# Performance work log

Hardware: AMD Instinct MI355X
Metric: run time of the kernel (lower is better)

The kernel has to match this reference:

```python
import jax, jax.numpy as jnp
import numpy as np

LEAKY_ALPHA = 0.2
NEG_INF = -9e15


def setup_inputs() -> dict:
    key = jax.random.key(0)
    k1, k2, k3, k4, k5 = jax.random.split(key, 5)
    n, n_head, f_in, f_out = 4096, 8, 1024, 128
    scale_w = float(np.sqrt(6.0 / (f_in + f_out)))      # xavier_uniform over (f_in,f_out)
    scale_a = float(np.sqrt(6.0 / (f_out + 1)))
    return {
        "h": jax.random.normal(k1, (n, f_in), dtype=jnp.float32),
        "adj": jax.random.randint(k2, (n, n), 0, 2, dtype=jnp.int32),
        "w": jax.random.uniform(k3, (n_head, f_in, f_out), jnp.float32, -scale_w, scale_w),
        "bias": jnp.zeros((f_out,), dtype=jnp.float32),
        "a_src": jax.random.uniform(k4, (n_head, f_out, 1), jnp.float32, -scale_a, scale_a),
        "a_dst": jax.random.uniform(k5, (n_head, f_out, 1), jnp.float32, -scale_a, scale_a),
    }


def reference(h, adj, w, bias, a_src, a_dst):
    n = h.shape[0]
    # per-head projection: [h_head, n, f_out]
    h_prime = jnp.einsum('nf,hfo->hno', h, w)
    attn_src = jnp.einsum('hno,hoi->hn', h_prime, a_src)   # [n_head, n]
    attn_dst = jnp.einsum('hno,hoi->hn', h_prime, a_dst)   # [n_head, n]
    # additive score: attn[h,i,j] = src[h,i] + dst[h,j]
    attn = attn_src[:, :, None] + attn_dst[:, None, :]
    attn = jnp.where(attn >= 0, attn, LEAKY_ALPHA * attn)  # leaky_relu
    attn = jnp.where(adj[None] > 0, attn, NEG_INF)
    attn = jax.nn.softmax(attn, axis=-1)                   # [n_head, n, n]
    # dropout layers are identity in eval mode
    output = jnp.einsum('hnm,hmo->hno', attn, h_prime) + bias
    output = jnp.transpose(output, (1, 0, 2)).reshape(n, -1)  # [n, n_head*f_out]
    weight = jnp.sum(attn, axis=0)                          # [n, n]
    return output, weight
```

## Files before the change

### kernel.cpp

```cpp
#include <hip/hip_runtime.h>
#include <hip/hip_bf16.h>


#define N 4096
#define NH 8
#define FIN 1024
#define FOUT 128

typedef short bf16x8 __attribute__((ext_vector_type(8)));
typedef float f32x4 __attribute__((ext_vector_type(4)));
typedef unsigned int uint;
typedef unsigned short ushort;

__device__ __forceinline__ float b2f(ushort u){ return __uint_as_float(((uint)u)<<16); }
__device__ __forceinline__ uint pk2cvt(float a, float b){
    float2 f; f.x=a; f.y=b;
    __hip_bfloat162 h = __float22bfloat162_rn(f);
    uint r; __builtin_memcpy(&r, &h, 4); return r;
}
__device__ __forceinline__ float sane(float x, float lim){ return fminf(fmaxf(x,-lim),lim); }
__device__ __forceinline__ int swz(int r, int cg){ return r*64 + (((cg) ^ (r & 7)) << 3); }
__device__ __forceinline__ void glds16(const ushort* g, ushort* l){
    __builtin_amdgcn_global_load_lds(
        (const __attribute__((address_space(1))) void*)g,
        (__attribute__((address_space(3))) void*)l, 16, 0, 0);
}
__device__ __forceinline__ int detect_mode(const ushort* hraw){
    ushort u = hraw[2*(threadIdx.x & 63)];
    int e = (u>>7)&0xFF;
    unsigned long long m = __ballot(e>=90 && e<=141);
    return (__popcll(m)>=40)?0:1;
}

__global__ __launch_bounds__(256) void pack_adj(const int* __restrict__ adj,
                                                uint* __restrict__ bitsT) {
    size_t idx = (size_t)blockIdx.x * 256 + threadIdx.x;
    int v = adj[idx];
    unsigned long long m = __ballot(v != 0);
    int lane = threadIdx.x & 63;
    uint i  = (uint)(idx >> 12);
    uint jw = ((uint)idx & 4095u) >> 5;
    if (lane == 0)       bitsT[jw * N + i] = (uint)m;
    else if (lane == 32) bitsT[jw * N + i] = (uint)(m >> 32);
}

__global__ __launch_bounds__(256) void transpose_w(const void* __restrict__ wraw,
                                                   const ushort* __restrict__ hraw,
                                                   ushort* __restrict__ wT) {
    __shared__ ushort tile[64][72];
    int mode = detect_mode(hraw);
    int h = blockIdx.z, f0 = blockIdx.x * 64, o0 = blockIdx.y * 64;
    int t = threadIdx.x;
#pragma unroll
    for (int it = 0; it < 2; ++it) {
        int slot = it * 256 + t;
        int row = slot >> 3, c = slot & 7;
        size_t eoff = (size_t)h * (FIN * FOUT) + (size_t)(f0 + row) * FOUT + o0 + c * 8;
        alignas(16) ushort tmp[8];
        if (mode == 0) {
            *reinterpret_cast<uint4*>(tmp) = *reinterpret_cast<const uint4*>((const ushort*)wraw + eoff);
        } else {
            const float* wF = (const float*)wraw;
            float4 x = *reinterpret_cast<const float4*>(wF + eoff);
            float4 y = *reinterpret_cast<const float4*>(wF + eoff + 4);
            uint4 p; p.x = pk2cvt(x.x,x.y); p.y = pk2cvt(x.z,x.w);
            p.z = pk2cvt(y.x,y.y); p.w = pk2cvt(y.z,y.w);
            *reinterpret_cast<uint4*>(tmp) = p;
        }
        *reinterpret_cast<uint4*>(&tile[row][c * 8]) = *reinterpret_cast<uint4*>(tmp);
    }
    __syncthreads();
#pragma unroll
    for (int it = 0; it < 2; ++it) {
        int slot = it * 256 + t;
        int orow = slot >> 3, c = slot & 7;
        alignas(16) ushort tmp[8];
#pragma unroll
        for (int k = 0; k < 8; ++k) tmp[k] = tile[c * 8 + k][orow];
        *reinterpret_cast<uint4*>(wT + (size_t)h * (FIN * FOUT) + (size_t)(o0 + orow) * FIN + f0 + c * 8) =
            *reinterpret_cast<uint4*>(tmp);
    }
}

__global__ __launch_bounds__(256) void zero2(float* __restrict__ acc, float* __restrict__ lsum,
                                             int nacc) {
    int b = blockIdx.x, t = threadIdx.x;
    float4 z; z.x=0.f; z.y=0.f; z.z=0.f; z.w=0.f;
    if (b < nacc) reinterpret_cast<float4*>(acc)[(size_t)b*256+t] = z;
    else          reinterpret_cast<float4*>(lsum)[(size_t)(b-nacc)*256+t] = z;
}

__global__ __launch_bounds__(256) void gemm_hp(
        const void* __restrict__ hraw, const ushort* __restrict__ wT,
        const void* __restrict__ asraw, const void* __restrict__ adraw,
        ushort* __restrict__ hpT,
        float* __restrict__ es1, float* __restrict__ es2,
        float* __restrict__ ed1, float* __restrict__ ed2) {
    __shared__ ushort Bs[2][FOUT * 64];
    __shared__ float sred[64], dred[64];
    int mode = detect_mode((const ushort*)hraw);
    int t = threadIdx.x;
    int lin = blockIdx.x + 64 * blockIdx.y;
    int i0 = (((lin & 7) * 8) + ((lin >> 6) & 7)) * 64;
    int head = (lin >> 3) & 7;
    int w = t >> 6, lane = t & 63, quad = lane >> 4, l16 = lane & 15, wsh = quad * 8;
    int arow = i0 + w * 16 + l16;
    const ushort* hU = (const ushort*)hraw;
    const float*  hF = (const float*)hraw;
    int l8 = lane >> 3, lk = (lane & 7) ^ (l8 & 7);
    const ushort* gs[4];
#pragma unroll
    for (int s = 0; s < 4; ++s) {
        int o = (w * 4 + s) * 8 + l8;
        gs[s] = wT + (size_t)head * FOUT * FIN + (size_t)o * FIN + lk * 8;
    }

    float asv[8], adv[8];
#pragma unroll
    for (int n = 0; n < 8; ++n) {
        int ai = head * FOUT + n * 16 + l16;
        asv[n] = mode ? ((const float*)asraw)[ai] : b2f(((const ushort*)asraw)[ai]);
        adv[n] = mode ? ((const float*)adraw)[ai] : b2f(((const ushort*)adraw)[ai]);
    }

    f32x4 acc[8] = {};
#pragma unroll
    for (int s = 0; s < 4; ++s) glds16(gs[s], &Bs[0][(w * 4 + s) * 512]);
    uint4 au[2]; float4 af[2][2];
    if (mode == 0) {
#pragma unroll
        for (int kk = 0; kk < 2; ++kk)
            au[kk] = *reinterpret_cast<const uint4*>(hU + (size_t)arow * FIN + kk * 32 + wsh);
    } else {
#pragma unroll
        for (int kk = 0; kk < 2; ++kk) {
            af[kk][0] = *reinterpret_cast<const float4*>(hF + (size_t)arow * FIN + kk * 32 + wsh);
            af[kk][1] = *reinterpret_cast<const float4*>(hF + (size_t)arow * FIN + kk * 32 + wsh + 4);
        }
    }
    __syncthreads();

    for (int c = 0; c < 16; ++c) {
        int k0 = c * 64;
        if (c < 15) {
            ushort* bsw = &Bs[(c + 1) & 1][0];
#pragma unroll
            for (int s = 0; s < 4; ++s)
                glds16(gs[s] + k0 + 64, &bsw[(w * 4 + s) * 512]);
        }
        bf16x8 a2[2];
        if (mode == 0) {
            a2[0] = *reinterpret_cast<bf16x8*>(&au[0]);
            a2[1] = *reinterpret_cast<bf16x8*>(&au[1]);
        } else {
#pragma unroll
            for (int kk = 0; kk < 2; ++kk) {
                uint4 av; av.x = pk2cvt(af[kk][0].x, af[kk][0].y); av.y = pk2cvt(af[kk][0].z, af[kk][0].w);
                av.z = pk2cvt(af[kk][1].x, af[kk][1].y); av.w = pk2cvt(af[kk][1].z, af[kk][1].w);
                a2[kk] = *reinterpret_cast<bf16x8*>(&av);
            }
        }
        if (c < 15) {
            if (mode == 0) {
#pragma unroll
                for (int kk = 0; kk < 2; ++kk)
                    au[kk] = *reinterpret_cast<const uint4*>(hU + (size_t)arow * FIN + k0 + 64 + kk * 32 + wsh);
            } else {
#pragma unroll
                for (int kk = 0; kk < 2; ++kk) {
                    af[kk][0] = *reinterpret_cast<const float4*>(hF + (size_t)arow * FIN + k0 + 64 + kk * 32 + wsh);
                    af[kk][1] = *reinterpret_cast<const float4*>(hF + (size_t)arow * FIN + k0 + 64 + kk * 32 + wsh + 4);
                }
            }
        }
        const ushort* bsr = &Bs[c & 1][0];
#pragma unroll
        for (int kk = 0; kk < 2; ++kk) {
            int cg0 = kk * 4 + quad;
#pragma unroll
            for (int n = 0; n < 8; ++n) {
                bf16x8 b = *reinterpret_cast<const bf16x8*>(&bsr[swz(n * 16 + l16, cg0)]);
                acc[n] = __builtin_amdgcn_mfma_f32_16x16x32_bf16(a2[kk], b, acc[n], 0, 0, 0);
            }
        }
        if (c < 15) __syncthreads();
    }
#pragma unroll
    for (int n = 0; n < 8; ++n) {
        uint2 pk;
        pk.x = pk2cvt(acc[n][0], acc[n][1]);
        pk.y = pk2cvt(acc[n][2], acc[n][3]);
        *reinterpret_cast<uint2*>(hpT + ((size_t)head * FOUT + n * 16 + l16) * N + i0 + w * 16 + quad * 4) = pk;
    }
#pragma unroll
    for (int rr = 0; rr < 4; ++rr) {
        float s = 0.f, d = 0.f;
#pragma unroll
        for (int n = 0; n < 8; ++n) { s += acc[n][rr] * asv[n]; d += acc[n][rr] * adv[n]; }
#pragma unroll
        for (int off = 1; off < 16; off <<= 1) { s += __shfl_xor(s, off); d += __shfl_xor(d, off); }
        if (l16 == 0) { sred[w * 16 + quad * 4 + rr] = s; dred[w * 16 + quad * 4 + rr] = d; }
    }
    __syncthreads();
    if (t < 64) {
        int i = i0 + t;
        float s = sane(sred[t], 30.f);
        float d = sane(dred[t], 30.f);
        es1[head * N + i] = __expf(s);       es2[head * N + i] = __expf(0.2f * s);
        ed1[head * N + i] = __expf(d);       ed2[head * N + i] = __expf(0.2f * d);
    }
}

__global__ __launch_bounds__(256, 4) void pv_kernel(
        const ushort* __restrict__ hpT,
        const float* __restrict__ es1, const float* __restrict__ es2,
        const float* __restrict__ ed1, const float* __restrict__ ed2,
        const uint* __restrict__ bitsT,
        float* __restrict__ accOut, float* __restrict__ lsum, int use_atomic) {
    __shared__ ushort Bs[2][FOUT * 64];
    __shared__ float Ed[2][1024];
    int t = threadIdx.x;
    int lin = blockIdx.x + 32 * blockIdx.y + 256 * blockIdx.z;
    int g  = (lin & 7) * 4 + (lin >> 8);
    int ib = (lin >> 3) & 31;
    int hh = g & 7, kz = g >> 3;
    int i0 = ib * 128, kb = kz * 1024;
    int w = t >> 6, lane = t & 63, quad = lane >> 4, l16 = lane & 15, wsh = quad * 8;
    int irow[2];
    float s1[2], s2[2];
#pragma unroll
    for (int mi = 0; mi < 2; ++mi) {
        irow[mi] = i0 + w * 32 + mi * 16 + l16;
        s1[mi] = es1[hh * N + irow[mi]];
        s2[mi] = es2[hh * N + irow[mi]];
    }
    const uint* bp = bitsT + (size_t)(kb >> 5) * N;
    int l8 = lane >> 3, lk = (lane & 7) ^ (l8 & 7);
    const ushort* gs[4];
#pragma unroll
    for (int s = 0; s < 4; ++s) {
        int o = (w * 4 + s) * 8 + l8;
        gs[s] = hpT + (size_t)hh * FOUT * N + (size_t)o * N + kb + lk * 8;
    }
    bf16x8 ones;
#pragma unroll
    for (int j = 0; j < 8; ++j) ones[j] = (short)0x3F80;

    f32x4 acc[2][8] = {};
    f32x4 accl[2] = {};

    float4 ev1 = *reinterpret_cast<const float4*>(ed1 + hh * N + kb + t * 4);
    float4 ev2 = *reinterpret_cast<const float4*>(ed2 + hh * N + kb + t * 4);
    uint bwc[2][2], bwn[2][2];
#pragma unroll
    for (int kk = 0; kk < 2; ++kk)
#pragma unroll
        for (int mi = 0; mi < 2; ++mi) bwc[kk][mi] = bp[(size_t)kk * N + irow[mi]];
#pragma unroll
    for (int s = 0; s < 4; ++s) glds16(gs[s], &Bs[0][(w * 4 + s) * 512]);
    *reinterpret_cast<float4*>(&Ed[0][t * 4]) = ev1;
    *reinterpret_cast<float4*>(&Ed[1][t * 4]) = ev2;
    __syncthreads();

    for (int c = 0; c < 16; ++c) {
        if (c < 15) {
            ushort* bsw = &Bs[(c + 1) & 1][0];
#pragma unroll
            for (int s = 0; s < 4; ++s)
                glds16(gs[s] + (c + 1) * 64, &bsw[(w * 4 + s) * 512]);
#pragma unroll
            for (int kk = 0; kk < 2; ++kk)
#pragma unroll
                for (int mi = 0; mi < 2; ++mi)
                    bwn[kk][mi] = bp[(size_t)((c + 1) * 2 + kk) * N + irow[mi]];
        }
        const ushort* bsr = &Bs[c & 1][0];
#pragma unroll
        for (int kk = 0; kk < 2; ++kk) {
            int kgl = c * 64 + kk * 32 + wsh;
            float4 d1a = *reinterpret_cast<const float4*>(&Ed[0][kgl]);
            float4 d1b = *reinterpret_cast<const float4*>(&Ed[0][kgl + 4]);
            float4 d2a = *reinterpret_cast<const float4*>(&Ed[1][kgl]);
            float4 d2b = *reinterpret_cast<const float4*>(&Ed[1][kgl + 4]);
            bf16x8 am[2];
#pragma unroll
            for (int mi = 0; mi < 2; ++mi) {
                uint word = bwc[kk][mi] >> wsh;
                float e0 = fmaxf(s1[mi]*d1a.x, s2[mi]*d2a.x); e0 = (word & 1u)   ? e0 : 0.f;
                float e1 = fmaxf(s1[mi]*d1a.y, s2[mi]*d2a.y); e1 = (word & 2u)   ? e1 : 0.f;
                float e2 = fmaxf(s1[mi]*d1a.z, s2[mi]*d2a.z); e2 = (word & 4u)   ? e2 : 0.f;
                float e3 = fmaxf(s1[mi]*d1a.w, s2[mi]*d2a.w); e3 = (word & 8u)   ? e3 : 0.f;
                float e4 = fmaxf(s1[mi]*d1b.x, s2[mi]*d2b.x); e4 = (word & 16u)  ? e4 : 0.f;
                float e5 = fmaxf(s1[mi]*d1b.y, s2[mi]*d2b.y); e5 = (word & 32u)  ? e5 : 0.f;
                float e6 = fmaxf(s1[mi]*d1b.z, s2[mi]*d2b.z); e6 = (word & 64u)  ? e6 : 0.f;
                float e7 = fmaxf(s1[mi]*d1b.w, s2[mi]*d2b.w); e7 = (word & 128u) ? e7 : 0.f;
                uint4 av; av.x = pk2cvt(e0, e1); av.y = pk2cvt(e2, e3);
                av.z = pk2cvt(e4, e5); av.w = pk2cvt(e6, e7);
                am[mi] = *reinterpret_cast<bf16x8*>(&av);
                accl[mi] = __builtin_amdgcn_mfma_f32_16x16x32_bf16(am[mi], ones, accl[mi], 0, 0, 0);
            }
            int cg0 = kk * 4 + quad;
            __builtin_amdgcn_s_setprio(1);
#pragma unroll
            for (int n = 0; n < 8; ++n) {
                bf16x8 b = *reinterpret_cast<const bf16x8*>(&bsr[swz(n * 16 + l16, cg0)]);
                acc[0][n] = __builtin_amdgcn_mfma_f32_16x16x32_bf16(am[0], b, acc[0][n], 0, 0, 0);
                acc[1][n] = __builtin_amdgcn_mfma_f32_16x16x32_bf16(am[1], b, acc[1][n], 0, 0, 0);
            }
            __builtin_amdgcn_s_setprio(0);
        }
#pragma unroll
        for (int kk = 0; kk < 2; ++kk)
#pragma unroll
            for (int mi = 0; mi < 2; ++mi) bwc[kk][mi] = bwn[kk][mi];
        if (c < 15) __syncthreads();
    }
    if (l16 == 0) {
#pragma unroll
        for (int mi = 0; mi < 2; ++mi)
#pragma unroll
            for (int rr = 0; rr < 4; ++rr)
                atomicAdd(&lsum[hh * N + i0 + w * 32 + mi * 16 + quad * 4 + rr], accl[mi][rr]);
    }
    if (use_atomic) {
#pragma unroll
        for (int mi = 0; mi < 2; ++mi) {
            float* arow = accOut + ((size_t)hh * N + i0 + w * 32 + mi * 16 + quad * 4) * FOUT + l16;
#pragma unroll
            for (int n = 0; n < 8; ++n)
#pragma unroll
                for (int rr = 0; rr < 4; ++rr)
                    atomicAdd(&arow[(size_t)rr * FOUT + n * 16], acc[mi][n][rr]);
        }
    } else {
        float* part = accOut + (size_t)kz * ((size_t)NH * N * FOUT);
#pragma unroll
        for (int mi = 0; mi < 2; ++mi) {
            float* arow = part + ((size_t)hh * N + i0 + w * 32 + mi * 16 + quad * 4) * FOUT + l16;
#pragma unroll
            for (int n = 0; n < 8; ++n)
#pragma unroll
                for (int rr = 0; rr < 4; ++rr)
                    arow[(size_t)rr * FOUT + n * 16] = acc[mi][n][rr];
        }
    }
}

__global__ __launch_bounds__(256) void recip2(const float* __restrict__ lsum,
                                              const float* __restrict__ es1, const float* __restrict__ es2,
                                              float* __restrict__ rinv,
                                              float* __restrict__ s1r, float* __restrict__ s2r) {
    int idx = blockIdx.x * 256 + threadIdx.x;
    float v = lsum[idx];
    float r = (v > 1e-30f) ? 1.0f / v : 0.f;
    rinv[idx] = r;
    s1r[idx] = es1[idx] * r;
    s2r[idx] = es2[idx] * r;
}

__global__ __launch_bounds__(256) void pv_epi(
        const float* __restrict__ acc32, const float* __restrict__ rinv,
        const void* __restrict__ braw, const ushort* __restrict__ hraw,
        void* __restrict__ outraw, int nparts) {
    int mode = detect_mode(hraw);
    int idx4 = blockIdx.x * 256 + threadIdx.x;
    int h = idx4 >> 17;
    int i = (idx4 >> 5) & 4095;
    int og = idx4 & 31;
    const size_t PSTRIDE4 = (size_t)NH * N * FOUT / 4;
    float4 v = reinterpret_cast<const float4*>(acc32)[idx4];
    if (nparts == 4) {
        float4 a = reinterpret_cast<const float4*>(acc32)[PSTRIDE4 + idx4];
        float4 b = reinterpret_cast<const float4*>(acc32)[2 * PSTRIDE4 + idx4];
        float4 c = reinterpret_cast<const float4*>(acc32)[3 * PSTRIDE4 + idx4];
        v.x += a.x + b.x + c.x; v.y += a.y + b.y + c.y;
        v.z += a.z + b.z + c.z; v.w += a.w + b.w + c.w;
    }
    float r = rinv[h * N + i];
    float4 bv;
    if (mode) bv = reinterpret_cast<const float4*>(braw)[og];
    else {
        const ushort* bu = (const ushort*)braw;
        bv.x = b2f(bu[og*4]); bv.y = b2f(bu[og*4+1]); bv.z = b2f(bu[og*4+2]); bv.w = b2f(bu[og*4+3]);
    }
    v.x = v.x * r + bv.x; v.y = v.y * r + bv.y; v.z = v.z * r + bv.z; v.w = v.w * r + bv.w;
    size_t ob = (size_t)i * (NH * FOUT) + h * FOUT + og * 4;
    if (mode) *reinterpret_cast<float4*>((float*)outraw + ob) = v;
    else {
        uint2 pk; pk.x = pk2cvt(v.x, v.y); pk.y = pk2cvt(v.z, v.w);
        *reinterpret_cast<uint2*>((ushort*)outraw + ob) = pk;
    }
}

__global__ __launch_bounds__(256) void weight_kernel(
        const float* __restrict__ s1r, const float* __restrict__ s2r,
        const float* __restrict__ ed1, const float* __restrict__ ed2,
        const uint* __restrict__ bitsT,
        const ushort* __restrict__ hraw,
        void* __restrict__ outraw) {
    int mode = detect_mode(hraw);
    ushort* woutU = (ushort*)outraw + (size_t)N * (NH * FOUT);
    float*  woutF = (float*)outraw  + (size_t)N * (NH * FOUT);
    int t = threadIdx.x;
    int j = blockIdx.x * 1024 + t * 4;
    int i0 = blockIdx.y * 32;
    float4 d1[NH], d2[NH];
#pragma unroll
    for (int hh = 0; hh < NH; ++hh) {
        d1[hh] = *reinterpret_cast<const float4*>(ed1 + hh * N + j);
        d2[hh] = *reinterpret_cast<const float4*>(ed2 + hh * N + j);
    }
    int wrow = j >> 5;
    int jsh = j & 31;
    for (int i = i0; i < i0 + 32; ++i) {
        uint wbits = bitsT[(size_t)wrow * N + i] >> jsh;
        float sx = 0.f, sy = 0.f, sz = 0.f, sw = 0.f;
#pragma unroll
        for (int hh = 0; hh < NH; ++hh) {
            float a = s1r[hh * N + i];
            float b = s2r[hh * N + i];
            sx += fmaxf(a * d1[hh].x, b * d2[hh].x);
            sy += fmaxf(a * d1[hh].y, b * d2[hh].y);
            sz += fmaxf(a * d1[hh].z, b * d2[hh].z);
            sw += fmaxf(a * d1[hh].w, b * d2[hh].w);
        }
        sx = (wbits & 1u) ? sx : 0.f;
        sy = (wbits & 2u) ? sy : 0.f;
        sz = (wbits & 4u) ? sz : 0.f;
        sw = (wbits & 8u) ? sw : 0.f;
        size_t oidx = (size_t)i * N + j;
        if (mode) {
            float4 st; st.x = sx; st.y = sy; st.z = sz; st.w = sw;
            *reinterpret_cast<float4*>(woutF + oidx) = st;
        } else {
            uint2 pk; pk.x = pk2cvt(sx, sy); pk.y = pk2cvt(sz, sw);
            *reinterpret_cast<uint2*>(woutU + oidx) = pk;
        }
    }
}

extern "C" void kernel_launch(void* const* d_in, const int* in_sizes, int n_in,
                              void* d_out, int out_size, void* d_ws, size_t ws_size,
                              hipStream_t stream) {
    (void)in_sizes; (void)n_in; (void)out_size;
    const void* hraw  = d_in[0];
    const int*  adj   = (const int*)d_in[1];
    const void* wraw  = d_in[2];
    const void* braw  = d_in[3];
    const void* asraw = d_in[4];
    const void* adraw = d_in[5];

    char* ws = (char*)d_ws;
    float* lsum = (float*)(ws + 0);
    float* rinv = (float*)(ws + 131072);
    float* es1  = (float*)(ws + 262144);
    float* es2  = (float*)(ws + 393216);
    float* ed1  = (float*)(ws + 524288);
    float* ed2  = (float*)(ws + 655360);
    float* s1r  = (float*)(ws + 786432);
    float* s2r  = (float*)(ws + 917504);
    uint*  bitsT= (uint*)(ws + 1048576);
    ushort* wT  = (ushort*)(ws + 3145728);

    const size_t SMALL_END = 5242880;
    const size_t PART = 16777216;
    float*  acc32; ushort* hpT;
    int use_atomic, nparts;
    if (ws_size >= SMALL_END + 4 * PART + 8388608ull) {
        char* b = ws + SMALL_END;
        acc32 = (float*)b;
        hpT   = (ushort*)(b + 4 * PART);
        use_atomic = 0; nparts = 4;
    } else if (ws_size >= SMALL_END + 25165824ull) {
        char* b = ws + SMALL_END;
        acc32 = (float*)b;
        hpT   = (ushort*)(b + PART);
        use_atomic = 1; nparts = 1;
    } else {
        char* ob = (char*)d_out;
        acc32 = (float*)(ob + 16777216);
        hpT   = (ushort*)(ob + 33554432);
        use_atomic = 1; nparts = 1;
    }

    transpose_w<<<dim3(16, 2, 8), 256, 0, stream>>>(wraw, (const ushort*)hraw, wT);
    pack_adj<<<65536, 256, 0, stream>>>(adj, bitsT);
    if (use_atomic) zero2<<<4128, 256, 0, stream>>>(acc32, lsum, 4096);
    else            zero2<<<32,   256, 0, stream>>>(acc32, lsum, 0);
    gemm_hp<<<dim3(64, 8), 256, 0, stream>>>(hraw, wT, asraw, adraw, hpT,
                                             es1, es2, ed1, ed2);
    pv_kernel<<<dim3(32, 8, 4), 256, 0, stream>>>(hpT, es1, es2, ed1, ed2, bitsT,
                                                  acc32, lsum, use_atomic);
    recip2<<<128, 256, 0, stream>>>(lsum, es1, es2, rinv, s1r, s2r);
    pv_epi<<<4096, 256, 0, stream>>>(acc32, rinv, braw, (const ushort*)hraw, d_out, nparts);
    weight_kernel<<<dim3(4, 128), 256, 0, stream>>>(s1r, s2r, ed1, ed2, bitsT,
                                                    (const ushort*)hraw, d_out);
}
```

Baseline: 290.0 us.

## Merge prep kernels, fold reciprocal into epilogue, pack score products

The adjacency packing, accumulator zeroing and weight transpose kernels become one launch with block-range dispatch. The standalone reciprocal kernel is folded into the output epilogue, which now computes the inverse row sum and writes the scaled source terms. In the PV kernel, the two destination exponent arrays are interleaved in shared memory so each score uses one packed v_pk_mul_f32 plus a max. The goal is fewer launches and fewer VALU instructions in the inner loop, at the cost of redundant reciprocal math across epilogue threads and inline asm that may hinder scheduling.

```diff
diff --git a/kernel.cpp b/kernel.cpp
--- a/kernel.cpp
+++ b/kernel.cpp
@@ -9,6 +9,7 @@
 
 typedef short bf16x8 __attribute__((ext_vector_type(8)));
 typedef float f32x4 __attribute__((ext_vector_type(4)));
+typedef float f32x2 __attribute__((ext_vector_type(2)));
 typedef unsigned int uint;
 typedef unsigned short ushort;
 
@@ -19,6 +20,11 @@
     uint r; __builtin_memcpy(&r, &h, 4); return r;
 }
 __device__ __forceinline__ float sane(float x, float lim){ return fminf(fmaxf(x,-lim),lim); }
+__device__ __forceinline__ float pkmulmax(f32x2 sp, f32x2 dp){
+    f32x2 pr;
+    asm("v_pk_mul_f32 %0, %1, %2" : "=v"(pr) : "v"(sp), "v"(dp));
+    return fmaxf(pr[0], pr[1]);
+}
 __device__ __forceinline__ int swz(int r, int cg){ return r*64 + (((cg) ^ (r & 7)) << 3); }
 __device__ __forceinline__ void glds16(const ushort* g, ushort* l){
     __builtin_amdgcn_global_load_lds(
@@ -32,25 +38,34 @@
     return (__popcll(m)>=40)?0:1;
 }
 
-__global__ __launch_bounds__(256) void pack_adj(const int* __restrict__ adj,
-                                                uint* __restrict__ bitsT) {
-    size_t idx = (size_t)blockIdx.x * 256 + threadIdx.x;
-    int v = adj[idx];
-    unsigned long long m = __ballot(v != 0);
-    int lane = threadIdx.x & 63;
-    uint i  = (uint)(idx >> 12);
-    uint jw = ((uint)idx & 4095u) >> 5;
-    if (lane == 0)       bitsT[jw * N + i] = (uint)m;
-    else if (lane == 32) bitsT[jw * N + i] = (uint)(m >> 32);
-}
-
-__global__ __launch_bounds__(256) void transpose_w(const void* __restrict__ wraw,
-                                                   const ushort* __restrict__ hraw,
-                                                   ushort* __restrict__ wT) {
+__global__ __launch_bounds__(256) void prep(
+        const int* __restrict__ adj, uint* __restrict__ bitsT,
+        float* __restrict__ acc, float* __restrict__ lsum, int nacc,
+        const void* __restrict__ wraw, const ushort* __restrict__ hraw,
+        ushort* __restrict__ wT) {
     __shared__ ushort tile[64][72];
+    int b = blockIdx.x, t = threadIdx.x;
+    if (b < 65536) {
+        size_t idx = (size_t)b * 256 + t;
+        int v = adj[idx];
+        unsigned long long m = __ballot(v != 0);
+        int lane = t & 63;
+        uint i  = (uint)(idx >> 12);
+        uint jw = ((uint)idx & 4095u) >> 5;
+        if (lane == 0)       bitsT[jw * N + i] = (uint)m;
+        else if (lane == 32) bitsT[jw * N + i] = (uint)(m >> 32);
+        return;
+    }
+    int zb = b - 65536;
+    if (zb < nacc + 32) {
+        float4 z; z.x=0.f; z.y=0.f; z.z=0.f; z.w=0.f;
+        if (zb < nacc) reinterpret_cast<float4*>(acc)[(size_t)zb*256+t] = z;
+        else           reinterpret_cast<float4*>(lsum)[(size_t)(zb-nacc)*256+t] = z;
+        return;
+    }
+    int bb = zb - (nacc + 32);
     int mode = detect_mode(hraw);
-    int h = blockIdx.z, f0 = blockIdx.x * 64, o0 = blockIdx.y * 64;
-    int t = threadIdx.x;
+    int f0 = (bb & 15) * 64, o0 = ((bb >> 4) & 1) * 64, h = bb >> 5;
 #pragma unroll
     for (int it = 0; it < 2; ++it) {
         int slot = it * 256 + t;
@@ -80,14 +95,6 @@
         *reinterpret_cast<uint4*>(wT + (size_t)h * (FIN * FOUT) + (size_t)(o0 + orow) * FIN + f0 + c * 8) =
             *reinterpret_cast<uint4*>(tmp);
     }
-}
-
-__global__ __launch_bounds__(256) void zero2(float* __restrict__ acc, float* __restrict__ lsum,
-                                             int nacc) {
-    int b = blockIdx.x, t = threadIdx.x;
-    float4 z; z.x=0.f; z.y=0.f; z.z=0.f; z.w=0.f;
-    if (b < nacc) reinterpret_cast<float4*>(acc)[(size_t)b*256+t] = z;
-    else          reinterpret_cast<float4*>(lsum)[(size_t)(b-nacc)*256+t] = z;
 }
 
 __global__ __launch_bounds__(256) void gemm_hp(
@@ -218,7 +225,7 @@
         const uint* __restrict__ bitsT,
         float* __restrict__ accOut, float* __restrict__ lsum, int use_atomic) {
     __shared__ ushort Bs[2][FOUT * 64];
-    __shared__ float Ed[2][1024];
+    __shared__ float Ed[2048];
     int t = threadIdx.x;
     int lin = blockIdx.x + 32 * blockIdx.y + 256 * blockIdx.z;
     int g  = (lin & 7) * 4 + (lin >> 8);
@@ -227,12 +234,12 @@
     int i0 = ib * 128, kb = kz * 1024;
     int w = t >> 6, lane = t & 63, quad = lane >> 4, l16 = lane & 15, wsh = quad * 8;
     int irow[2];
-    float s1[2], s2[2];
+    f32x2 sp[2];
 #pragma unroll
     for (int mi = 0; mi < 2; ++mi) {
         irow[mi] = i0 + w * 32 + mi * 16 + l16;
-        s1[mi] = es1[hh * N + irow[mi]];
-        s2[mi] = es2[hh * N + irow[mi]];
+        sp[mi][0] = es1[hh * N + irow[mi]];
+        sp[mi][1] = es2[hh * N + irow[mi]];
     }
     const uint* bp = bitsT + (size_t)(kb >> 5) * N;
     int l8 = lane >> 3, lk = (lane & 7) ^ (l8 & 7);
@@ -258,8 +265,15 @@
         for (int mi = 0; mi < 2; ++mi) bwc[kk][mi] = bp[(size_t)kk * N + irow[mi]];
 #pragma unroll
     for (int s = 0; s < 4; ++s) glds16(gs[s], &Bs[0][(w * 4 + s) * 512]);
-    *reinterpret_cast<float4*>(&Ed[0][t * 4]) = ev1;
-    *reinterpret_cast<float4*>(&Ed[1][t * 4]) = ev2;
+    {
+        const float* e1a = reinterpret_cast<const float*>(&ev1);
+        const float* e2a = reinterpret_cast<const float*>(&ev2);
+#pragma unroll
+        for (int j = 0; j < 4; ++j) {
+            float2 pr; pr.x = e1a[j]; pr.y = e2a[j];
+            *reinterpret_cast<float2*>(&Ed[(t * 4 + j) * 2]) = pr;
+        }
+    }
     __syncthreads();
 
     for (int c = 0; c < 16; ++c) {
@@ -277,23 +291,23 @@
         const ushort* bsr = &Bs[c & 1][0];
 #pragma unroll
         for (int kk = 0; kk < 2; ++kk) {
-            int kgl = c * 64 + kk * 32 + wsh;
-            float4 d1a = *reinterpret_cast<const float4*>(&Ed[0][kgl]);
-            float4 d1b = *reinterpret_cast<const float4*>(&Ed[0][kgl + 4]);
-            float4 d2a = *reinterpret_cast<const float4*>(&Ed[1][kgl]);
-            float4 d2b = *reinterpret_cast<const float4*>(&Ed[1][kgl + 4]);
+            int eb = (c * 64 + kk * 32 + wsh) * 2;
+            float4 p01 = *reinterpret_cast<const float4*>(&Ed[eb]);
+            float4 p23 = *reinterpret_cast<const float4*>(&Ed[eb + 4]);
+            float4 p45 = *reinterpret_cast<const float4*>(&Ed[eb + 8]);
+            float4 p67 = *reinterpret_cast<const float4*>(&Ed[eb + 12]);
             bf16x8 am[2];
 #pragma unroll
             for (int mi = 0; mi < 2; ++mi) {
                 uint word = bwc[kk][mi] >> wsh;
-                float e0 = fmaxf(s1[mi]*d1a.x, s2[mi]*d2a.x); e0 = (word & 1u)   ? e0 : 0.f;
-                float e1 = fmaxf(s1[mi]*d1a.y, s2[mi]*d2a.y); e1 = (word & 2u)   ? e1 : 0.f;
-                float e2 = fmaxf(s1[mi]*d1a.z, s2[mi]*d2a.z); e2 = (word & 4u)   ? e2 : 0.f;
-                float e3 = fmaxf(s1[mi]*d1a.w, s2[mi]*d2a.w); e3 = (word & 8u)   ? e3 : 0.f;
-                float e4 = fmaxf(s1[mi]*d1b.x, s2[mi]*d2b.x); e4 = (word & 16u)  ? e4 : 0.f;
-                float e5 = fmaxf(s1[mi]*d1b.y, s2[mi]*d2b.y); e5 = (word & 32u)  ? e5 : 0.f;
-                float e6 = fmaxf(s1[mi]*d1b.z, s2[mi]*d2b.z); e6 = (word & 64u)  ? e6 : 0.f;
-                float e7 = fmaxf(s1[mi]*d1b.w, s2[mi]*d2b.w); e7 = (word & 128u) ? e7 : 0.f;
+                float e0 = pkmulmax(sp[mi], *reinterpret_cast<const f32x2*>(&p01.x)); e0 = (word & 1u)   ? e0 : 0.f;
+                float e1 = pkmulmax(sp[mi], *reinterpret_cast<const f32x2*>(&p01.z)); e1 = (word & 2u)   ? e1 : 0.f;
+                float e2 = pkmulmax(sp[mi], *reinterpret_cast<const f32x2*>(&p23.x)); e2 = (word & 4u)   ? e2 : 0.f;
+                float e3 = pkmulmax(sp[mi], *reinterpret_cast<const f32x2*>(&p23.z)); e3 = (word & 8u)   ? e3 : 0.f;
+                float e4 = pkmulmax(sp[mi], *reinterpret_cast<const f32x2*>(&p45.x)); e4 = (word & 16u)  ? e4 : 0.f;
+                float e5 = pkmulmax(sp[mi], *reinterpret_cast<const f32x2*>(&p45.z)); e5 = (word & 32u)  ? e5 : 0.f;
+                float e6 = pkmulmax(sp[mi], *reinterpret_cast<const f32x2*>(&p67.x)); e6 = (word & 64u)  ? e6 : 0.f;
+                float e7 = pkmulmax(sp[mi], *reinterpret_cast<const f32x2*>(&p67.z)); e7 = (word & 128u) ? e7 : 0.f;
                 uint4 av; av.x = pk2cvt(e0, e1); av.y = pk2cvt(e2, e3);
                 av.z = pk2cvt(e4, e5); av.w = pk2cvt(e6, e7);
                 am[mi] = *reinterpret_cast<bf16x8*>(&av);
@@ -346,22 +360,12 @@
     }
 }
 
-__global__ __launch_bounds__(256) void recip2(const float* __restrict__ lsum,
-                                              const float* __restrict__ es1, const float* __restrict__ es2,
-                                              float* __restrict__ rinv,
-                                              float* __restrict__ s1r, float* __restrict__ s2r) {
-    int idx = blockIdx.x * 256 + threadIdx.x;
-    float v = lsum[idx];
-    float r = (v > 1e-30f) ? 1.0f / v : 0.f;
-    rinv[idx] = r;
-    s1r[idx] = es1[idx] * r;
-    s2r[idx] = es2[idx] * r;
-}
-
 __global__ __launch_bounds__(256) void pv_epi(
-        const float* __restrict__ acc32, const float* __restrict__ rinv,
+        const float* __restrict__ acc32, const float* __restrict__ lsum,
+        const float* __restrict__ es1, const float* __restrict__ es2,
         const void* __restrict__ braw, const ushort* __restrict__ hraw,
-        void* __restrict__ outraw, int nparts) {
+        void* __restrict__ outraw,
+        float* __restrict__ s1r, float* __restrict__ s2r, int nparts) {
     int mode = detect_mode(hraw);
     int idx4 = blockIdx.x * 256 + threadIdx.x;
     int h = idx4 >> 17;
@@ -376,7 +380,12 @@
         v.x += a.x + b.x + c.x; v.y += a.y + b.y + c.y;
         v.z += a.z + b.z + c.z; v.w += a.w + b.w + c.w;
     }
-    float r = rinv[h * N + i];
+    float lv = lsum[h * N + i];
+    float r = (lv > 1e-30f) ? 1.0f / lv : 0.f;
+    if (og == 0) {
+        s1r[h * N + i] = es1[h * N + i] * r;
+        s2r[h * N + i] = es2[h * N + i] * r;
+    }
     float4 bv;
     if (mode) bv = reinterpret_cast<const float4*>(braw)[og];
     else {
@@ -452,7 +461,6 @@
 
     char* ws = (char*)d_ws;
     float* lsum = (float*)(ws + 0);
-    float* rinv = (float*)(ws + 131072);
     float* es1  = (float*)(ws + 262144);
     float* es2  = (float*)(ws + 393216);
     float* ed1  = (float*)(ws + 524288);
@@ -483,16 +491,15 @@
         use_atomic = 1; nparts = 1;
     }
 
-    transpose_w<<<dim3(16, 2, 8), 256, 0, stream>>>(wraw, (const ushort*)hraw, wT);
-    pack_adj<<<65536, 256, 0, stream>>>(adj, bitsT);
-    if (use_atomic) zero2<<<4128, 256, 0, stream>>>(acc32, lsum, 4096);
-    else            zero2<<<32,   256, 0, stream>>>(acc32, lsum, 0);
+    int nacc = use_atomic ? 4096 : 0;
+    prep<<<65536 + nacc + 32 + 256, 256, 0, stream>>>(adj, bitsT, acc32, lsum, nacc,
+                                                      wraw, (const ushort*)hraw, wT);
     gemm_hp<<<dim3(64, 8), 256, 0, stream>>>(hraw, wT, asraw, adraw, hpT,
                                              es1, es2, ed1, ed2);
     pv_kernel<<<dim3(32, 8, 4), 256, 0, stream>>>(hpT, es1, es2, ed1, ed2, bitsT,
                                                   acc32, lsum, use_atomic);
-    recip2<<<128, 256, 0, stream>>>(lsum, es1, es2, rinv, s1r, s2r);
-    pv_epi<<<4096, 256, 0, stream>>>(acc32, rinv, braw, (const ushort*)hraw, d_out, nparts);
+    pv_epi<<<4096, 256, 0, stream>>>(acc32, lsum, es1, es2, braw, (const ushort*)hraw,
+                                     d_out, s1r, s2r, nparts);
     weight_kernel<<<dim3(4, 128), 256, 0, stream>>>(s1r, s2r, ed1, ed2, bitsT,
                                                     (const ushort*)hraw, d_out);
 }
```

Result: no change. 293.9 us (+1.4%).
